# Performance work log

Hardware: AMD Instinct MI355X
Metric: run time of the kernel (lower is better)

## Reference

```python
import jax, jax.numpy as jnp
import numpy as np

EMBED_DIM = 1024
NUM_HEADS = 8
SEQ_LEN = 2048
EPS = 1e-6


def setup_inputs() -> dict:
    key = jax.random.key(0)
    ks = jax.random.split(key, 8)
    E, NH, S = EMBED_DIM, NUM_HEADS, SEQ_LEN
    q = jax.random.normal(ks[0], (S, E), jnp.float32)
    k = jax.random.normal(ks[1], (S, E), jnp.float32)
    v = jax.random.normal(ks[2], (S, E), jnp.float32)
    # gate projections: weights init'd to zeros in the module; use small random
    # values so the gate math is exercised. Biases follow the module's init.
    Wi = 0.02 * jax.random.normal(ks[3], (NH, 3 * E), jnp.float32)
    bi = jnp.linspace(3.0, 6.0, NH, dtype=jnp.float32)
    Wf = 0.02 * jax.random.normal(ks[4], (NH, 3 * E), jnp.float32)
    bf = jnp.sqrt(0.1) * jax.random.normal(ks[5], (NH,), jnp.float32)
    # ResidualLayerNorm (xLSTM-style): effective scale = 1 + weight, no bias
    ln_weight = jnp.zeros((E,), jnp.float32)
    return {"q": q, "k": k, "v": v, "Wi": Wi, "bi": bi, "Wf": Wf, "bf": bf,
            "ln_weight": ln_weight}


def _mlstm_parallel(q, k, v, Wi, bi, Wf, bf, ln_weight):
    S, E = q.shape
    NH = Wi.shape[0]
    DH = E // NH
    gate_in = jnp.concatenate((q, k, v), axis=1)            # (S, 3E)
    ig = (gate_in @ Wi.T + bi).T[:, :, None]                # (NH, S, 1)
    fg = (gate_in @ Wf.T + bf).T[:, :, None]                # (NH, S, 1)

    qh = q.reshape(S, NH, DH).transpose(1, 0, 2)            # (NH, S, DH)
    kh = k.reshape(S, NH, DH).transpose(1, 0, 2)
    vh = v.reshape(S, NH, DH).transpose(1, 0, 2)

    # cumulative log forget gates
    log_f = jax.nn.log_sigmoid(fg)                          # (NH, S, 1)
    log_f_cum = jnp.concatenate(
        [jnp.zeros((NH, 1, 1), q.dtype), jnp.cumsum(log_f, axis=1)], axis=1
    )                                                       # (NH, S+1, 1)
    log_fg_mat = log_f_cum - log_f_cum.transpose(0, 2, 1)   # (NH, S+1, S+1)
    causal = jnp.tril(jnp.ones((S, S), bool))
    log_fg_mat = jnp.where(causal, log_fg_mat[:, 1:, 1:], -jnp.inf)  # (NH,S,S)

    log_D = log_fg_mat + ig.transpose(0, 2, 1)              # (NH, S, S)
    max_log_D = jnp.max(log_D, axis=-1, keepdims=True)      # (NH, S, 1)
    D = jnp.exp(log_D - max_log_D)                          # stabilized

    qk = jnp.einsum('hsd,htd->hst', qh, kh) / jnp.sqrt(jnp.asarray(DH, q.dtype))
    C = qk * D                                              # (NH, S, S)
    normalizer = jnp.maximum(jnp.abs(jnp.sum(C, axis=-1, keepdims=True)),
                             jnp.exp(-max_log_D))
    C_norm = C / (normalizer + EPS)
    h = jnp.einsum('hst,htd->hsd', C_norm, vh)              # (NH, S, DH)
    h = h.transpose(1, 0, 2).reshape(S, E)

    # residual layer norm: LN(h) * (1 + weight), no bias
    mu = jnp.mean(h, axis=-1, keepdims=True)
    var = jnp.mean(jnp.square(h - mu), axis=-1, keepdims=True)
    h_norm = (h - mu) * jax.lax.rsqrt(var + 1e-5)
    return h_norm * (1.0 + ln_weight)


def reference(q, k, v, Wi, bi, Wf, bf, ln_weight):
    return _mlstm_parallel(q, k, v, Wi, bi, Wf, bf, ln_weight)
```

## Files before the change

kernel.cpp:

```cpp
#include <hip/hip_runtime.h>
#include <math.h>

#define S_LEN 2048
#define EMB   1024
#define NHEAD 8
#define DH    128
#define E3    3072
#define BM    64
#define BN    32
#define NSPLIT 4
#define PTSTRIDE 40

typedef __bf16 bf16x8 __attribute__((ext_vector_type(8)));
typedef __bf16 bf16x4 __attribute__((ext_vector_type(4)));
typedef float  f32x4  __attribute__((ext_vector_type(4)));

__device__ __forceinline__ void gload16(const __bf16* g, __bf16* l) {
    __builtin_amdgcn_global_load_lds(
        (const __attribute__((address_space(1))) void*)g,
        (__attribute__((address_space(3))) void*)l, 16, 0, 0);
}

__global__ __launch_bounds__(256) void gates_cvt_transpose_kernel(
    const float* __restrict__ q, const float* __restrict__ k,
    const float* __restrict__ v,
    const float* __restrict__ Wi, const float* __restrict__ bi,
    const float* __restrict__ Wf, const float* __restrict__ bf,
    __bf16* __restrict__ Qh, __bf16* __restrict__ Ql,
    __bf16* __restrict__ Kh, __bf16* __restrict__ Kl,
    __bf16* __restrict__ Vt,
    float* __restrict__ ig, float* __restrict__ lf)
{
    const int tid = threadIdx.x;
    __shared__ union {
        float red[16][4];
        __bf16 tile[32][33];
    } sh;

    if (blockIdx.x < S_LEN) {
        const int t = blockIdx.x;
        const float4 qv = ((const float4*)q)[(size_t)t * 256 + tid];
        const float4 kv = ((const float4*)k)[(size_t)t * 256 + tid];
        const float4 vv = ((const float4*)v)[(size_t)t * 256 + tid];
        {
            size_t idx = (size_t)t * 256 + tid;
            bf16x4 hi, lo;
            hi[0]=(__bf16)qv.x; hi[1]=(__bf16)qv.y; hi[2]=(__bf16)qv.z; hi[3]=(__bf16)qv.w;
            lo[0]=(__bf16)(qv.x-(float)hi[0]); lo[1]=(__bf16)(qv.y-(float)hi[1]);
            lo[2]=(__bf16)(qv.z-(float)hi[2]); lo[3]=(__bf16)(qv.w-(float)hi[3]);
            ((bf16x4*)Qh)[idx] = hi; ((bf16x4*)Ql)[idx] = lo;
            hi[0]=(__bf16)kv.x; hi[1]=(__bf16)kv.y; hi[2]=(__bf16)kv.z; hi[3]=(__bf16)kv.w;
            lo[0]=(__bf16)(kv.x-(float)hi[0]); lo[1]=(__bf16)(kv.y-(float)hi[1]);
            lo[2]=(__bf16)(kv.z-(float)hi[2]); lo[3]=(__bf16)(kv.w-(float)hi[3]);
            ((bf16x4*)Kh)[idx] = hi; ((bf16x4*)Kl)[idx] = lo;
        }
        float acc[16];
        #pragma unroll
        for (int g = 0; g < 16; ++g) {
            const float4* w4 = (const float4*)((g < 8) ? (Wi + g * E3) : (Wf + (g - 8) * E3));
            float4 a = w4[tid], b = w4[256 + tid], c = w4[512 + tid];
            acc[g] = a.x*qv.x + a.y*qv.y + a.z*qv.z + a.w*qv.w
                   + b.x*kv.x + b.y*kv.y + b.z*kv.z + b.w*kv.w
                   + c.x*vv.x + c.y*vv.y + c.z*vv.z + c.w*vv.w;
        }
        const int w = tid >> 6, lane = tid & 63;
        #pragma unroll
        for (int g = 0; g < 16; ++g) {
            float x = acc[g];
            for (int o = 32; o > 0; o >>= 1) x += __shfl_down(x, o, 64);
            if (lane == 0) sh.red[g][w] = x;
        }
        __syncthreads();
        if (tid < 16) {
            float s = sh.red[tid][0] + sh.red[tid][1] + sh.red[tid][2] + sh.red[tid][3];
            if (tid < 8) {
                ig[tid * S_LEN + t] = s + bi[tid];
            } else {
                int h = tid - 8;
                float x = s + bf[h];
                lf[h * S_LEN + t] = fminf(x, 0.f) - log1pf(expf(-fabsf(x)));
            }
        }
    } else {
        const int tb = blockIdx.x - S_LEN;
        const int sb = (tb & 63) * 32, eb = (tb >> 6) * 32;
        #pragma unroll
        for (int i = 0; i < 4; ++i) {
            int lin = tid + i * 256;
            int sr = lin >> 5, ec = lin & 31;
            sh.tile[ec][sr] = (__bf16)v[(size_t)(sb + sr) * EMB + eb + ec];
        }
        __syncthreads();
        #pragma unroll
        for (int i = 0; i < 4; ++i) {
            int lin = tid + i * 256;
            int er = lin >> 5, sc = lin & 31;
            Vt[(size_t)(eb + er) * S_LEN + sb + sc] = sh.tile[er][sc];
        }
    }
}

__global__ __launch_bounds__(256) void cumsum_aux_kernel(
    const float* __restrict__ lf, const float* __restrict__ ig,
    float* __restrict__ F, float* __restrict__ ug,
    float* __restrict__ umax, float* __restrict__ upmax)
{
    const int h = blockIdx.x, tid = threadIdx.x;
    const int lane = tid & 63, w = tid >> 6;
    __shared__ float wsum[4];
    __shared__ float morig[256];
    float loc[8];
    const int base = tid * 8;
    float s = 0.f;
    for (int i = 0; i < 8; i++) { s += lf[h * S_LEN + base + i]; loc[i] = s; }
    float inc = s;
    #pragma unroll
    for (int o = 1; o < 64; o <<= 1) {
        float t = __shfl_up(inc, o, 64);
        if (lane >= o) inc += t;
    }
    if (lane == 63) wsum[w] = inc;
    __syncthreads();
    float wpre = 0.f;
    #pragma unroll
    for (int i = 0; i < 4; ++i) if (i < w) wpre += wsum[i];
    const float prev = wpre + inc - s;
    float* Fh = F + h * (S_LEN + 1);
    if (tid == 0) Fh[0] = 0.f;
    float Fv[8];
    for (int i = 0; i < 8; i++) { Fv[i] = prev + loc[i]; Fh[base + i + 1] = Fv[i]; }

    const float* igh = ig + h * S_LEN;
    float pm[8];
    float runm = -1e30f;
    #pragma unroll
    for (int i = 0; i < 8; i++) {
        float u = igh[base + i] - Fv[i];
        ug[h * S_LEN + base + i] = u;
        runm = fmaxf(runm, u);
        pm[i] = runm;
    }
    morig[tid] = runm;
    __syncthreads();
    const int g0 = tid & ~3;
    float pfx = -1e30f;
    for (int j = g0; j < tid; ++j) pfx = fmaxf(pfx, morig[j]);
    #pragma unroll
    for (int i = 0; i < 8; i++)
        upmax[h * S_LEN + base + i] = fmaxf(pfx, pm[i]);
    if ((tid & 3) == 0) {
        float mm = fmaxf(fmaxf(morig[tid], morig[tid + 1]),
                         fmaxf(morig[tid + 2], morig[tid + 3]));
        umax[h * 64 + (tid >> 2)] = mm;
    }
}

__global__ __launch_bounds__(256, 2) void mlstm_mfma(
    const __bf16* __restrict__ Qhg, const __bf16* __restrict__ Qlg,
    const __bf16* __restrict__ Khg, const __bf16* __restrict__ Klg,
    const __bf16* __restrict__ Vtg,
    const float* __restrict__ ug, const float* __restrict__ umaxg,
    const float* __restrict__ upmaxg, const float* __restrict__ F,
    __bf16* __restrict__ Opart, float* __restrict__ msplit,
    float* __restrict__ lsplit)
{
    const int flat = blockIdx.x;
    const int h = flat & 7;
    const int rest = flat >> 3;
    const int xx = rest & 15, z = rest >> 4;
    const int tid  = threadIdx.x;
    const int lane = tid & 63, w = tid >> 6;
    const int quad = lane >> 4, l15 = lane & 15;

    __shared__ __bf16 KhL[2][4096];
    __shared__ __bf16 KlL[2][4096];
    __shared__ __bf16 VtL[2][4096];
    __shared__ __bf16 Pt[4][16 * PTSTRIDE];

    const float* Fh  = F  + h * (S_LEN + 1);
    const float* ugh = ug + h * S_LEN;
    const float scale = 0.088388347648318447f;

    const int krow0 = tid >> 4;
    const int krow1 = 16 + krow0;
    const int kchk  = (tid & 15) ^ (krow0 & 15);
    const int vrow0 = tid >> 2;
    const int vrow1 = 64 + vrow0;
    const int vchk  = (tid & 3) ^ ((vrow0 ^ (vrow0 >> 2)) & 3);
    const int ldsw  = w * 512;

#define STAGE(B, TB) do {                                                     \
    const __bf16* kb_ = Khg + (size_t)(TB) * EMB + h * DH;                    \
    const __bf16* lb_ = Klg + (size_t)(TB) * EMB + h * DH;                    \
    const __bf16* vg_ = Vtg + (size_t)(h * DH) * S_LEN + (TB);                \
    gload16(kb_ + (size_t)krow0 * EMB + kchk * 8, &KhL[B][ldsw]);             \
    gload16(kb_ + (size_t)krow1 * EMB + kchk * 8, &KhL[B][2048 + ldsw]);      \
    gload16(lb_ + (size_t)krow0 * EMB + kchk * 8, &KlL[B][ldsw]);             \
    gload16(lb_ + (size_t)krow1 * EMB + kchk * 8, &KlL[B][2048 + ldsw]);      \
    gload16(vg_ + (size_t)vrow0 * S_LEN + vchk * 8, &VtL[B][ldsw]);           \
    gload16(vg_ + (size_t)vrow1 * S_LEN + vchk * 8, &VtL[B][2048 + ldsw]);    \
} while (0)

    for (int pair = 0; pair < 2; ++pair) {
        const int qt = (pair == 0) ? xx : 31 - xx;
        const int qb = qt * BM;
        const int nj = 2 * qt + 2;
        const int j0 = (z * nj) / NSPLIT, j1 = ((z + 1) * nj) / NSPLIT;
        const int qbw = qb + w * 16;
        const int SBLK = (qb >> 5) + (w >> 1);

        float fq[4], upm[4];
        int sglob[4];
        #pragma unroll
        for (int r = 0; r < 4; ++r) {
            int s = qbw + quad * 4 + r;
            sglob[r] = s;
            fq[r]  = Fh[s + 1];
            upm[r] = upmaxg[h * S_LEN + s];
        }

        bf16x8 qh[4], ql[4];
        {
            const size_t qrow = (size_t)(qbw + l15) * EMB + h * DH + quad * 8;
            #pragma unroll
            for (int kk = 0; kk < 4; ++kk) {
                qh[kk] = *(const bf16x8*)(Qhg + qrow + kk * 32);
                ql[kk] = *(const bf16x8*)(Qlg + qrow + kk * 32);
            }
        }
        #pragma unroll
        for (int kk = 0; kk < 4; ++kk)
            asm volatile("" : "+v"(qh[kk]), "+v"(ql[kk]));

        float m_r[4] = {-1e30f, -1e30f, -1e30f, -1e30f};
        float l_r[4] = {0.f, 0.f, 0.f, 0.f};
        f32x4 Oacc[8] = {{0,0,0,0},{0,0,0,0},{0,0,0,0},{0,0,0,0},
                         {0,0,0,0},{0,0,0,0},{0,0,0,0},{0,0,0,0}};

        float pu0 = 0.f, pu1 = 0.f, pum = 0.f;
        int buf = 0;
        if (j0 < j1) {
            STAGE(0, j0 * BN);
            pu0 = ugh[j0 * BN + l15];
            pu1 = ugh[j0 * BN + 16 + l15];
            pum = umaxg[h * 64 + j0];
            __syncthreads();
        }

        for (int j = j0; j < j1; ++j) {
            const int tb = j * BN;
            const float ut0 = pu0, ut1 = pu1, umj = pum;
            if (j + 1 < j1) {
                STAGE(buf ^ 1, tb + BN);
                pu0 = ugh[tb + BN + l15];
                pu1 = ugh[tb + BN + 16 + l15];
                pum = umaxg[h * 64 + (j + 1)];
            }
            if (j <= SBLK) {
                f32x4 S0 = {0,0,0,0}, S1 = {0,0,0,0};
                #pragma unroll
                for (int kk = 0; kk < 4; ++kk) {
                    const int kpos = (((kk << 2) | quad) ^ l15) * 8;
                    bf16x8 bh0 = *(const bf16x8*)&KhL[buf][l15 * 128 + kpos];
                    bf16x8 bl0 = *(const bf16x8*)&KlL[buf][l15 * 128 + kpos];
                    S0 = __builtin_amdgcn_mfma_f32_16x16x32_bf16(qh[kk], bh0, S0, 0, 0, 0);
                    S0 = __builtin_amdgcn_mfma_f32_16x16x32_bf16(qh[kk], bl0, S0, 0, 0, 0);
                    S0 = __builtin_amdgcn_mfma_f32_16x16x32_bf16(ql[kk], bh0, S0, 0, 0, 0);
                    bf16x8 bh1 = *(const bf16x8*)&KhL[buf][(16 + l15) * 128 + kpos];
                    bf16x8 bl1 = *(const bf16x8*)&KlL[buf][(16 + l15) * 128 + kpos];
                    S1 = __builtin_amdgcn_mfma_f32_16x16x32_bf16(qh[kk], bh1, S1, 0, 0, 0);
                    S1 = __builtin_amdgcn_mfma_f32_16x16x32_bf16(qh[kk], bl1, S1, 0, 0, 0);
                    S1 = __builtin_amdgcn_mfma_f32_16x16x32_bf16(ql[kk], bh1, S1, 0, 0, 0);
                }
                const int t0 = tb + l15, t1 = tb + 16 + l15;
                #pragma unroll
                for (int r = 0; r < 4; ++r) {
                    float mt = (j < SBLK) ? (fq[r] + umj) : (fq[r] + upm[r]);
                    float mn = fmaxf(m_r[r], mt);
                    float alpha = __expf(m_r[r] - mn);
                    m_r[r] = mn;
                    #pragma unroll
                    for (int nt = 0; nt < 8; ++nt) Oacc[nt][r] *= alpha;
                    float p0 = __expf(fq[r] + ut0 - mn) * S0[r] * scale;
                    float p1 = __expf(fq[r] + ut1 - mn) * S1[r] * scale;
                    if (j == SBLK) {
                        if (t0 > sglob[r]) p0 = 0.f;
                        if (t1 > sglob[r]) p1 = 0.f;
                    }
                    l_r[r] = l_r[r] * alpha + (p0 + p1);
                    const int prow = (quad * 4 + r) * PTSTRIDE;
                    Pt[w][prow + l15]      = (__bf16)p0;
                    Pt[w][prow + 16 + l15] = (__bf16)p1;
                }
                bf16x8 pa = *(const bf16x8*)&Pt[w][l15 * PTSTRIDE + quad * 8];
                #pragma unroll
                for (int nt = 0; nt < 8; ++nt) {
                    const int vrow = nt * 16 + l15;
                    const int vpos = (quad ^ ((vrow ^ (vrow >> 2)) & 3)) * 8;
                    bf16x8 vv = *(const bf16x8*)&VtL[buf][vrow * 32 + vpos];
                    Oacc[nt] = __builtin_amdgcn_mfma_f32_16x16x32_bf16(pa, vv, Oacc[nt], 0, 0, 0);
                }
            }
            __syncthreads();
            buf ^= 1;
        }
        __bf16* Oz = Opart + (size_t)z * S_LEN * EMB;
        #pragma unroll
        for (int nt = 0; nt < 8; ++nt) {
            #pragma unroll
            for (int r = 0; r < 4; ++r) {
                Oz[(size_t)sglob[r] * EMB + h * DH + nt * 16 + l15] = (__bf16)Oacc[nt][r];
            }
        }
        #pragma unroll
        for (int r = 0; r < 4; ++r) {
            float x = l_r[r];
            #pragma unroll
            for (int o = 1; o < 16; o <<= 1) x += __shfl_xor(x, o);
            l_r[r] = x;
        }
        if (l15 == 0) {
            #pragma unroll
            for (int r = 0; r < 4; ++r) {
                msplit[(z * NHEAD + h) * S_LEN + sglob[r]] = m_r[r];
                lsplit[(z * NHEAD + h) * S_LEN + sglob[r]] = l_r[r];
            }
        }
    }
#undef STAGE
}

__global__ __launch_bounds__(256) void combine_ln_kernel(
    const __bf16* __restrict__ Opart, const float* __restrict__ msplit,
    const float* __restrict__ lsplit, const float* __restrict__ lnw,
    float* __restrict__ out)
{
    const int tid = threadIdx.x;
    const int r  = tid >> 7;
    const int wr = (tid >> 6) & 1;
    const int c0 = (tid & 127) * 8;
    const int hh = c0 >> 7;
    const int s  = blockIdx.x * 2 + r;
    __shared__ float redsum[2][2], redvar[2][2];

    float m = -1e30f, es[NSPLIT], l = 0.f;
    #pragma unroll
    for (int zz = 0; zz < NSPLIT; ++zz)
        m = fmaxf(m, msplit[(zz * NHEAD + hh) * S_LEN + s]);
    #pragma unroll
    for (int zz = 0; zz < NSPLIT; ++zz) {
        es[zz] = __expf(msplit[(zz * NHEAD + hh) * S_LEN + s] - m);
        l += es[zz] * lsplit[(zz * NHEAD + hh) * S_LEN + s];
    }
    const float rn = 1.f / (fmaxf(fabsf(l), __expf(-m)) + 1e-6f);

    const size_t SE = (size_t)S_LEN * EMB;
    float x[8] = {0,0,0,0,0,0,0,0};
    #pragma unroll
    for (int zz = 0; zz < NSPLIT; ++zz) {
        if (es[zz] != 0.f) {
            bf16x8 o = *(const bf16x8*)(Opart + zz * SE + (size_t)s * EMB + c0);
            #pragma unroll
            for (int e = 0; e < 8; ++e) x[e] += es[zz] * (float)o[e];
        }
    }
    float sum = 0.f;
    #pragma unroll
    for (int e = 0; e < 8; ++e) { x[e] *= rn; sum += x[e]; }
    for (int o = 32; o > 0; o >>= 1) sum += __shfl_down(sum, o, 64);
    if ((tid & 63) == 0) redsum[r][wr] = sum;
    __syncthreads();
    sum = redsum[r][0] + redsum[r][1];
    const float mu = sum * (1.f / EMB);
    float vs = 0.f;
    #pragma unroll
    for (int e = 0; e < 8; ++e) { float d = x[e] - mu; vs += d * d; }
    for (int o = 32; o > 0; o >>= 1) vs += __shfl_down(vs, o, 64);
    if ((tid & 63) == 0) redvar[r][wr] = vs;
    __syncthreads();
    vs = redvar[r][0] + redvar[r][1];
    const float rstd = rsqrtf(vs * (1.f / EMB) + 1e-5f);
    const float4 w0 = *(const float4*)(lnw + c0);
    const float4 w1 = *(const float4*)(lnw + c0 + 4);
    float4 o0, o1;
    o0.x = (x[0]-mu)*rstd*(1.f+w0.x); o0.y = (x[1]-mu)*rstd*(1.f+w0.y);
    o0.z = (x[2]-mu)*rstd*(1.f+w0.z); o0.w = (x[3]-mu)*rstd*(1.f+w0.w);
    o1.x = (x[4]-mu)*rstd*(1.f+w1.x); o1.y = (x[5]-mu)*rstd*(1.f+w1.y);
    o1.z = (x[6]-mu)*rstd*(1.f+w1.z); o1.w = (x[7]-mu)*rstd*(1.f+w1.w);
    *(float4*)(out + (size_t)s * EMB + c0)     = o0;
    *(float4*)(out + (size_t)s * EMB + c0 + 4) = o1;
}

extern "C" void kernel_launch(void* const* d_in, const int* in_sizes, int n_in,
                              void* d_out, int out_size, void* d_ws, size_t ws_size,
                              hipStream_t stream)
{
    const float* q   = (const float*)d_in[0];
    const float* k   = (const float*)d_in[1];
    const float* v   = (const float*)d_in[2];
    const float* Wi  = (const float*)d_in[3];
    const float* bi  = (const float*)d_in[4];
    const float* Wf  = (const float*)d_in[5];
    const float* bf  = (const float*)d_in[6];
    const float* lnw = (const float*)d_in[7];
    float* out = (float*)d_out;

    float* ws = (float*)d_ws;
    float* ig    = ws;
    float* lf    = ig + NHEAD * S_LEN;
    float* F     = lf + NHEAD * S_LEN;
    float* ugw   = F + NHEAD * (S_LEN + 1);
    float* umaxw = ugw + NHEAD * S_LEN;
    float* upmaxw= umaxw + NHEAD * 64;
    __bf16* Qh = (__bf16*)(upmaxw + NHEAD * S_LEN);
    const size_t SEb = (size_t)S_LEN * EMB;
    __bf16* Ql  = Qh + SEb;
    __bf16* Kh  = Ql + SEb;
    __bf16* Kl  = Kh + SEb;
    __bf16* Vtg = Kl + SEb;
    __bf16* Opart = Vtg + SEb;
    float* msplit = (float*)(Opart + (size_t)NSPLIT * SEb);
    float* lsplit = msplit + NSPLIT * NHEAD * S_LEN;

    gates_cvt_transpose_kernel<<<2 * S_LEN, 256, 0, stream>>>(
        q, k, v, Wi, bi, Wf, bf, Qh, Ql, Kh, Kl, Vtg, ig, lf);
    cumsum_aux_kernel<<<NHEAD, 256, 0, stream>>>(lf, ig, F, ugw, umaxw, upmaxw);
    mlstm_mfma<<<16 * NHEAD * NSPLIT, 256, 0, stream>>>(
        Qh, Ql, Kh, Kl, Vtg, ugw, umaxw, upmaxw, F, Opart, msplit, lsplit);
    combine_ln_kernel<<<S_LEN / 2, 256, 0, stream>>>(Opart, msplit, lsplit, lnw, out);
}
```

Before: 155.9 us.

## Compute gate projections with split-K bf16x3 MFMA GEMM; single-buffer V tile

Moves the gate projection (S x 3E times 3E x 16) out of the per-row scalar dot-product blocks into a separate set of split-K blocks that use bf16 hi/lo triple MFMA. Partial sums are written to a workspace and reduced, together with bias and log-sigmoid, inside the cumsum kernel. The main attention kernel also single-buffers the V tile in LDS, issuing its load at the start of each iteration and adding an extra barrier before the PV matmul. This frees LDS, at the cost of exposing V load latency, and the cumsum kernel now does more serial reads.

```diff
diff --git a/kernel.cpp b/kernel.cpp
--- a/kernel.cpp
+++ b/kernel.cpp
@@ -9,6 +9,9 @@
 #define BM    64
 #define BN    32
 #define NSPLIT 4
+#define KSPLIT 8
+#define KCH   (E3 / KSPLIT)
+#define NGEMM (32 * KSPLIT)
 #define PTSTRIDE 40
 
 typedef __bf16 bf16x8 __attribute__((ext_vector_type(8)));
@@ -21,87 +24,89 @@
         (__attribute__((address_space(3))) void*)l, 16, 0, 0);
 }
 
-__global__ __launch_bounds__(256) void gates_cvt_transpose_kernel(
+__global__ __launch_bounds__(256) void gates_gemm_cvt_trans_kernel(
     const float* __restrict__ q, const float* __restrict__ k,
     const float* __restrict__ v,
-    const float* __restrict__ Wi, const float* __restrict__ bi,
-    const float* __restrict__ Wf, const float* __restrict__ bf,
+    const float* __restrict__ Wi, const float* __restrict__ Wf,
     __bf16* __restrict__ Qh, __bf16* __restrict__ Ql,
     __bf16* __restrict__ Kh, __bf16* __restrict__ Kl,
-    __bf16* __restrict__ Vt,
-    float* __restrict__ ig, float* __restrict__ lf)
+    __bf16* __restrict__ Vt, float* __restrict__ gpart)
 {
     const int tid = threadIdx.x;
-    __shared__ union {
-        float red[16][4];
-        __bf16 tile[32][33];
-    } sh;
-
-    if (blockIdx.x < S_LEN) {
-        const int t = blockIdx.x;
+    const int bid = blockIdx.x;
+    __shared__ __bf16 tile[32][33];
+
+    if (bid < NGEMM) {
+        const int tt = bid >> 3, ks = bid & (KSPLIT - 1);
+        const int w = tid >> 6, lane = tid & 63;
+        const int quad = lane >> 4, l15 = lane & 15;
+        const int tbase = tt * 64 + w * 16;
+        const float* wrow = (l15 < 8) ? (Wi + l15 * E3) : (Wf + (l15 - 8) * E3);
+        f32x4 acc = {0.f, 0.f, 0.f, 0.f};
+        #pragma unroll
+        for (int j = 0; j < KCH / 32; ++j) {
+            const int K0 = ks * KCH + j * 32;
+            const float* src; int off;
+            if (K0 < 1024)      { src = q; off = K0; }
+            else if (K0 < 2048) { src = k; off = K0 - 1024; }
+            else                { src = v; off = K0 - 2048; }
+            const float* ap = src + (size_t)(tbase + l15) * EMB + off + quad * 8;
+            float4 a0 = *(const float4*)ap,       a1 = *(const float4*)(ap + 4);
+            const float* bp = wrow + K0 + quad * 8;
+            float4 b0 = *(const float4*)bp,       b1 = *(const float4*)(bp + 4);
+            float af[8] = {a0.x,a0.y,a0.z,a0.w,a1.x,a1.y,a1.z,a1.w};
+            float bfv[8] = {b0.x,b0.y,b0.z,b0.w,b1.x,b1.y,b1.z,b1.w};
+            bf16x8 ah, al, bh, bl;
+            #pragma unroll
+            for (int e = 0; e < 8; ++e) {
+                __bf16 ha = (__bf16)af[e];
+                ah[e] = ha; al[e] = (__bf16)(af[e] - (float)ha);
+                __bf16 hb = (__bf16)bfv[e];
+                bh[e] = hb; bl[e] = (__bf16)(bfv[e] - (float)hb);
+            }
+            acc = __builtin_amdgcn_mfma_f32_16x16x32_bf16(ah, bh, acc, 0, 0, 0);
+            acc = __builtin_amdgcn_mfma_f32_16x16x32_bf16(ah, bl, acc, 0, 0, 0);
+            acc = __builtin_amdgcn_mfma_f32_16x16x32_bf16(al, bh, acc, 0, 0, 0);
+        }
+        float* gp = gpart + (size_t)(ks * 16 + l15) * S_LEN + tbase;
+        #pragma unroll
+        for (int r = 0; r < 4; ++r) gp[quad * 4 + r] = acc[r];
+    } else if (bid < NGEMM + S_LEN) {
+        const int t = bid - NGEMM;
         const float4 qv = ((const float4*)q)[(size_t)t * 256 + tid];
         const float4 kv = ((const float4*)k)[(size_t)t * 256 + tid];
-        const float4 vv = ((const float4*)v)[(size_t)t * 256 + tid];
-        {
-            size_t idx = (size_t)t * 256 + tid;
-            bf16x4 hi, lo;
-            hi[0]=(__bf16)qv.x; hi[1]=(__bf16)qv.y; hi[2]=(__bf16)qv.z; hi[3]=(__bf16)qv.w;
-            lo[0]=(__bf16)(qv.x-(float)hi[0]); lo[1]=(__bf16)(qv.y-(float)hi[1]);
-            lo[2]=(__bf16)(qv.z-(float)hi[2]); lo[3]=(__bf16)(qv.w-(float)hi[3]);
-            ((bf16x4*)Qh)[idx] = hi; ((bf16x4*)Ql)[idx] = lo;
-            hi[0]=(__bf16)kv.x; hi[1]=(__bf16)kv.y; hi[2]=(__bf16)kv.z; hi[3]=(__bf16)kv.w;
-            lo[0]=(__bf16)(kv.x-(float)hi[0]); lo[1]=(__bf16)(kv.y-(float)hi[1]);
-            lo[2]=(__bf16)(kv.z-(float)hi[2]); lo[3]=(__bf16)(kv.w-(float)hi[3]);
-            ((bf16x4*)Kh)[idx] = hi; ((bf16x4*)Kl)[idx] = lo;
-        }
-        float acc[16];
-        #pragma unroll
-        for (int g = 0; g < 16; ++g) {
-            const float4* w4 = (const float4*)((g < 8) ? (Wi + g * E3) : (Wf + (g - 8) * E3));
-            float4 a = w4[tid], b = w4[256 + tid], c = w4[512 + tid];
-            acc[g] = a.x*qv.x + a.y*qv.y + a.z*qv.z + a.w*qv.w
-                   + b.x*kv.x + b.y*kv.y + b.z*kv.z + b.w*kv.w
-                   + c.x*vv.x + c.y*vv.y + c.z*vv.z + c.w*vv.w;
-        }
-        const int w = tid >> 6, lane = tid & 63;
-        #pragma unroll
-        for (int g = 0; g < 16; ++g) {
-            float x = acc[g];
-            for (int o = 32; o > 0; o >>= 1) x += __shfl_down(x, o, 64);
-            if (lane == 0) sh.red[g][w] = x;
-        }
-        __syncthreads();
-        if (tid < 16) {
-            float s = sh.red[tid][0] + sh.red[tid][1] + sh.red[tid][2] + sh.red[tid][3];
-            if (tid < 8) {
-                ig[tid * S_LEN + t] = s + bi[tid];
-            } else {
-                int h = tid - 8;
-                float x = s + bf[h];
-                lf[h * S_LEN + t] = fminf(x, 0.f) - log1pf(expf(-fabsf(x)));
-            }
-        }
+        size_t idx = (size_t)t * 256 + tid;
+        bf16x4 hi, lo;
+        hi[0]=(__bf16)qv.x; hi[1]=(__bf16)qv.y; hi[2]=(__bf16)qv.z; hi[3]=(__bf16)qv.w;
+        lo[0]=(__bf16)(qv.x-(float)hi[0]); lo[1]=(__bf16)(qv.y-(float)hi[1]);
+        lo[2]=(__bf16)(qv.z-(float)hi[2]); lo[3]=(__bf16)(qv.w-(float)hi[3]);
+        ((bf16x4*)Qh)[idx] = hi; ((bf16x4*)Ql)[idx] = lo;
+        hi[0]=(__bf16)kv.x; hi[1]=(__bf16)kv.y; hi[2]=(__bf16)kv.z; hi[3]=(__bf16)kv.w;
+        lo[0]=(__bf16)(kv.x-(float)hi[0]); lo[1]=(__bf16)(kv.y-(float)hi[1]);
+        lo[2]=(__bf16)(kv.z-(float)hi[2]); lo[3]=(__bf16)(kv.w-(float)hi[3]);
+        ((bf16x4*)Kh)[idx] = hi; ((bf16x4*)Kl)[idx] = lo;
     } else {
-        const int tb = blockIdx.x - S_LEN;
+        const int tb = bid - NGEMM - S_LEN;
         const int sb = (tb & 63) * 32, eb = (tb >> 6) * 32;
         #pragma unroll
         for (int i = 0; i < 4; ++i) {
             int lin = tid + i * 256;
             int sr = lin >> 5, ec = lin & 31;
-            sh.tile[ec][sr] = (__bf16)v[(size_t)(sb + sr) * EMB + eb + ec];
+            tile[ec][sr] = (__bf16)v[(size_t)(sb + sr) * EMB + eb + ec];
         }
         __syncthreads();
         #pragma unroll
         for (int i = 0; i < 4; ++i) {
             int lin = tid + i * 256;
             int er = lin >> 5, sc = lin & 31;
-            Vt[(size_t)(eb + er) * S_LEN + sb + sc] = sh.tile[er][sc];
+            Vt[(size_t)(eb + er) * S_LEN + sb + sc] = tile[er][sc];
         }
     }
 }
 
 __global__ __launch_bounds__(256) void cumsum_aux_kernel(
-    const float* __restrict__ lf, const float* __restrict__ ig,
+    const float* __restrict__ gpart,
+    const float* __restrict__ bi, const float* __restrict__ bfp,
     float* __restrict__ F, float* __restrict__ ug,
     float* __restrict__ umax, float* __restrict__ upmax)
 {
@@ -109,10 +114,23 @@
     const int lane = tid & 63, w = tid >> 6;
     __shared__ float wsum[4];
     __shared__ float morig[256];
-    float loc[8];
+    const float bih = bi[h], bfh = bfp[h];
+    float loc[8], igv[8];
     const int base = tid * 8;
     float s = 0.f;
-    for (int i = 0; i < 8; i++) { s += lf[h * S_LEN + base + i]; loc[i] = s; }
+    for (int i = 0; i < 8; i++) {
+        const int t = base + i;
+        float ri = 0.f, rf = 0.f;
+        #pragma unroll
+        for (int ks = 0; ks < KSPLIT; ++ks) {
+            ri += gpart[(size_t)(ks * 16 + h) * S_LEN + t];
+            rf += gpart[(size_t)(ks * 16 + 8 + h) * S_LEN + t];
+        }
+        igv[i] = ri + bih;
+        float x = rf + bfh;
+        float lfv = fminf(x, 0.f) - log1pf(expf(-fabsf(x)));
+        s += lfv; loc[i] = s;
+    }
     float inc = s;
     #pragma unroll
     for (int o = 1; o < 64; o <<= 1) {
@@ -130,12 +148,11 @@
     float Fv[8];
     for (int i = 0; i < 8; i++) { Fv[i] = prev + loc[i]; Fh[base + i + 1] = Fv[i]; }
 
-    const float* igh = ig + h * S_LEN;
     float pm[8];
     float runm = -1e30f;
     #pragma unroll
     for (int i = 0; i < 8; i++) {
-        float u = igh[base + i] - Fv[i];
+        float u = igv[i] - Fv[i];
         ug[h * S_LEN + base + i] = u;
         runm = fmaxf(runm, u);
         pm[i] = runm;
@@ -174,7 +191,7 @@
 
     __shared__ __bf16 KhL[2][4096];
     __shared__ __bf16 KlL[2][4096];
-    __shared__ __bf16 VtL[2][4096];
+    __shared__ __bf16 VtL[4096];
     __shared__ __bf16 Pt[4][16 * PTSTRIDE];
 
     const float* Fh  = F  + h * (S_LEN + 1);
@@ -189,16 +206,18 @@
     const int vchk  = (tid & 3) ^ ((vrow0 ^ (vrow0 >> 2)) & 3);
     const int ldsw  = w * 512;
 
-#define STAGE(B, TB) do {                                                     \
+#define STAGE_K(B, TB) do {                                                   \
     const __bf16* kb_ = Khg + (size_t)(TB) * EMB + h * DH;                    \
     const __bf16* lb_ = Klg + (size_t)(TB) * EMB + h * DH;                    \
-    const __bf16* vg_ = Vtg + (size_t)(h * DH) * S_LEN + (TB);                \
     gload16(kb_ + (size_t)krow0 * EMB + kchk * 8, &KhL[B][ldsw]);             \
     gload16(kb_ + (size_t)krow1 * EMB + kchk * 8, &KhL[B][2048 + ldsw]);      \
     gload16(lb_ + (size_t)krow0 * EMB + kchk * 8, &KlL[B][ldsw]);             \
     gload16(lb_ + (size_t)krow1 * EMB + kchk * 8, &KlL[B][2048 + ldsw]);      \
-    gload16(vg_ + (size_t)vrow0 * S_LEN + vchk * 8, &VtL[B][ldsw]);           \
-    gload16(vg_ + (size_t)vrow1 * S_LEN + vchk * 8, &VtL[B][2048 + ldsw]);    \
+} while (0)
+#define STAGE_V(TB) do {                                                      \
+    const __bf16* vg_ = Vtg + (size_t)(h * DH) * S_LEN + (TB);                \
+    gload16(vg_ + (size_t)vrow0 * S_LEN + vchk * 8, &VtL[ldsw]);              \
+    gload16(vg_ + (size_t)vrow1 * S_LEN + vchk * 8, &VtL[2048 + ldsw]);       \
 } while (0)
 
     for (int pair = 0; pair < 2; ++pair) {
@@ -240,7 +259,7 @@
         float pu0 = 0.f, pu1 = 0.f, pum = 0.f;
         int buf = 0;
         if (j0 < j1) {
-            STAGE(0, j0 * BN);
+            STAGE_K(0, j0 * BN);
             pu0 = ugh[j0 * BN + l15];
             pu1 = ugh[j0 * BN + 16 + l15];
             pum = umaxg[h * 64 + j0];
@@ -249,9 +268,10 @@
 
         for (int j = j0; j < j1; ++j) {
             const int tb = j * BN;
+            STAGE_V(tb);
+            if (j + 1 < j1) STAGE_K(buf ^ 1, tb + BN);
             const float ut0 = pu0, ut1 = pu1, umj = pum;
             if (j + 1 < j1) {
-                STAGE(buf ^ 1, tb + BN);
                 pu0 = ugh[tb + BN + l15];
                 pu1 = ugh[tb + BN + 16 + l15];
                 pum = umaxg[h * 64 + (j + 1)];
@@ -292,12 +312,15 @@
                     Pt[w][prow + l15]      = (__bf16)p0;
                     Pt[w][prow + 16 + l15] = (__bf16)p1;
                 }
+            }
+            __syncthreads();
+            if (j <= SBLK) {
                 bf16x8 pa = *(const bf16x8*)&Pt[w][l15 * PTSTRIDE + quad * 8];
                 #pragma unroll
                 for (int nt = 0; nt < 8; ++nt) {
                     const int vrow = nt * 16 + l15;
                     const int vpos = (quad ^ ((vrow ^ (vrow >> 2)) & 3)) * 8;
-                    bf16x8 vv = *(const bf16x8*)&VtL[buf][vrow * 32 + vpos];
+                    bf16x8 vv = *(const bf16x8*)&VtL[vrow * 32 + vpos];
                     Oacc[nt] = __builtin_amdgcn_mfma_f32_16x16x32_bf16(pa, vv, Oacc[nt], 0, 0, 0);
                 }
             }
@@ -327,7 +350,8 @@
             }
         }
     }
-#undef STAGE
+#undef STAGE_K
+#undef STAGE_V
 }
 
 __global__ __launch_bounds__(256) void combine_ln_kernel(
@@ -406,9 +430,8 @@
     float* out = (float*)d_out;
 
     float* ws = (float*)d_ws;
-    float* ig    = ws;
-    float* lf    = ig + NHEAD * S_LEN;
-    float* F     = lf + NHEAD * S_LEN;
+    float* gpart = ws;
+    float* F     = gpart + KSPLIT * 16 * S_LEN;
     float* ugw   = F + NHEAD * (S_LEN + 1);
     float* umaxw = ugw + NHEAD * S_LEN;
     float* upmaxw= umaxw + NHEAD * 64;
@@ -422,9 +445,10 @@
     float* msplit = (float*)(Opart + (size_t)NSPLIT * SEb);
     float* lsplit = msplit + NSPLIT * NHEAD * S_LEN;
 
-    gates_cvt_transpose_kernel<<<2 * S_LEN, 256, 0, stream>>>(
-        q, k, v, Wi, bi, Wf, bf, Qh, Ql, Kh, Kl, Vtg, ig, lf);
-    cumsum_aux_kernel<<<NHEAD, 256, 0, stream>>>(lf, ig, F, ugw, umaxw, upmaxw);
+    gates_gemm_cvt_trans_kernel<<<NGEMM + S_LEN + 2048, 256, 0, stream>>>(
+        q, k, v, Wi, Wf, Qh, Ql, Kh, Kl, Vtg, gpart);
+    cumsum_aux_kernel<<<NHEAD, 256, 0, stream>>>(
+        gpart, bi, bf, F, ugw, umaxw, upmaxw);
     mlstm_mfma<<<16 * NHEAD * NSPLIT, 256, 0, stream>>>(
         Qh, Ql, Kh, Kl, Vtg, ugw, umaxw, upmaxw, F, Opart, msplit, lsplit);
     combine_ln_kernel<<<S_LEN / 2, 256, 0, stream>>>(Opart, msplit, lsplit, lnw, out);
```

After: 147.4 us. -5.4%, faster.
